# Kernel optimization log

Measured on AMD Instinct MI355X. Metric: run time of the kernel, lower is better.

The kernel has to match this reference:

```python
import jax, jax.numpy as jnp
import numpy as np

silu = jax.nn.silu
B, L, H, IN = 128, 2048, 8, 37
NL = 8  # 4 encoder + 4 decoder SE3 layers, stacked


def _se3_layer(h, pos, eW1, eb1, eW2, eb2, pW1, pb1, pW2, nW1, nb1, nW2, nb2):
    # chain graph: row = 0..N-2, col = 1..N-1 (as in the torch arange edges)
    rel = pos[1:] - pos[:-1]                      # [N-1, 3]
    dist = jnp.linalg.norm(rel, axis=-1, keepdims=True)
    ef = jnp.concatenate([h[:-1], h[1:], dist], axis=-1)   # [N-1, 2H+1]
    ea = silu(ef @ eW1 + eb1) @ eW2 + eb2                   # edge_mlp
    dp = silu(ea @ pW1 + pb1) @ pW2                         # pos_mlp (no bias on last)
    pos_upd = jnp.zeros_like(pos).at[:-1].add(dp).at[1:].add(-dp)
    node_upd = jnp.zeros_like(h).at[:-1].add(ea).at[1:].add(ea)
    h_out = silu(jnp.concatenate([h, node_upd], axis=-1) @ nW1 + nb1) @ nW2 + nb2
    return h_out, pos + 0.1 * pos_upd


def setup_inputs() -> dict:
    key = jax.random.key(0)
    ks = jax.random.split(key, 64)
    i = iter(range(64))
    def p(shape, s=0.1):
        return (jax.random.normal(ks[next(i)], shape, jnp.float32) * s)
    inp = {
        "atom_positions": jax.random.normal(ks[next(i)], (B, L, IN, 3), jnp.float32),
        "atom_mask": (jax.random.uniform(ks[next(i)], (B, L, IN)) < 0.8).astype(jnp.float32),
        "emb_W": p((IN, H)), "emb_b": p((H,)),
        "posemb_W1": p((3, H)), "posemb_b1": p((H,)),
        "posemb_W2": p((H, H)), "posemb_b2": p((H,)),
        # stacked SE3 conv params: layers 0-3 encoder, 4-7 decoder
        "conv_eW1": p((NL, 2 * H + 1, H)), "conv_eb1": p((NL, H)),
        "conv_eW2": p((NL, H, H)), "conv_eb2": p((NL, H)),
        "conv_pW1": p((NL, H, H)), "conv_pb1": p((NL, H)),
        "conv_pW2": p((NL, H, 3)),
        "conv_nW1": p((NL, 2 * H, H)), "conv_nb1": p((NL, H)),
        "conv_nW2": p((NL, H, H)), "conv_nb2": p((NL, H)),
        "tol_W1": p((H, H)), "tol_b1": p((H,)),
        "tol_W2": p((H, H)), "tol_b2": p((H,)),
        "froml_W1": p((H, H)), "froml_b1": p((H,)),
        "froml_W2": p((H, H)), "froml_b2": p((H,)),
        "posdec_W1": p((H, 2 * H)), "posdec_b1": p((2 * H,)),
        "posdec_W2": p((2 * H, IN * 3)), "posdec_b2": p((IN * 3,)),
        "maskdec_W": p((H, IN)), "maskdec_b": p((IN,)),
    }
    return inp


def reference(atom_positions, atom_mask, emb_W, emb_b, posemb_W1, posemb_b1,
              posemb_W2, posemb_b2, conv_eW1, conv_eb1, conv_eW2, conv_eb2,
              conv_pW1, conv_pb1, conv_pW2, conv_nW1, conv_nb1, conv_nW2,
              conv_nb2, tol_W1, tol_b1, tol_W2, tol_b2, froml_W1, froml_b1,
              froml_W2, froml_b2, posdec_W1, posdec_b1, posdec_W2, posdec_b2,
              maskdec_W, maskdec_b):
    # ---- encode ----
    h = atom_mask @ emb_W + emb_b                              # [B,L,H]
    m = atom_mask[..., None]
    mean_pos = (atom_positions * m).sum(axis=2) / (m.sum(axis=2) + 1e-8)  # [B,L,3]
    pos_feat = silu(mean_pos @ posemb_W1 + posemb_b1) @ posemb_W2 + posemb_b2
    h = (h + pos_feat).reshape(B * L, H)
    pos = mean_pos.reshape(B * L, 3)
    for li in range(4):
        h, pos = _se3_layer(h, pos, conv_eW1[li], conv_eb1[li], conv_eW2[li],
                            conv_eb2[li], conv_pW1[li], conv_pb1[li], conv_pW2[li],
                            conv_nW1[li], conv_nb1[li], conv_nW2[li], conv_nb2[li])
    h = h.reshape(B, L, H)
    z = silu(h @ tol_W1 + tol_b1) @ tol_W2 + tol_b2            # [B,L,latent]
    # ---- decode ----
    h = silu(z @ froml_W1 + froml_b1) @ froml_W2 + froml_b2
    h = h.reshape(B * L, H)
    pos = pos  # already flat [B*L, 3]
    for li in range(4, 8):
        h, pos = _se3_layer(h, pos, conv_eW1[li], conv_eb1[li], conv_eW2[li],
                            conv_eb2[li], conv_pW1[li], conv_pb1[li], conv_pW2[li],
                            conv_nW1[li], conv_nb1[li], conv_nW2[li], conv_nb2[li])
    h = h.reshape(B, L, H)
    pos_out = (silu(h @ posdec_W1 + posdec_b1) @ posdec_W2 + posdec_b2)
    pos_out = pos_out.reshape(B, L, IN, 3)
    mask_out = h @ maskdec_W + maskdec_b                       # [B,L,IN]
    return pos_out, mask_out
```

## Files before the change

### kernel.cpp

```cpp
#include <hip/hip_runtime.h>

#define NTOT 262144
#define NLAY 8
#define SEGOUT 48
#define NSEG ((NTOT + SEGOUT - 1) / SEGOUT)

__device__ __forceinline__ float silu_f(float x) {
    return x * __builtin_amdgcn_rcpf(1.0f + __expf(-x));
}

__global__ __launch_bounds__(256) void k_encode(
    const float* __restrict__ ap, const float* __restrict__ amask,
    const float* __restrict__ embW, const float* __restrict__ embB,
    const float* __restrict__ peW1, const float* __restrict__ peB1,
    const float* __restrict__ peW2, const float* __restrict__ peB2,
    float* __restrict__ h0, float* __restrict__ pos0)
{
    __shared__ alignas(16) float sM[64 * 37];
    __shared__ alignas(16) float sA[64 * 111];
    __shared__ alignas(16) float sW[37 * 8];
    const int tid = threadIdx.x;
    const long nb = (long)blockIdx.x * 64;

    if (tid < 74) ((float4*)sW)[tid] = ((const float4*)embW)[tid];
    const float4* gm = (const float4*)(amask + nb * 37);
    float4* sm4 = (float4*)sM;
    #pragma unroll 1
    for (int i = tid; i < 64 * 37 / 4; i += 256) sm4[i] = gm[i];
    const float4* ga = (const float4*)(ap + nb * 111);
    float4* sa4 = (float4*)sA;
    #pragma unroll 1
    for (int i = tid; i < 64 * 111 / 4; i += 256) sa4[i] = ga[i];
    __syncthreads();

    const int n = tid >> 2;
    const int p = tid & 3;
    const int k0 = p * 10;
    const int k1 = (p == 3) ? 37 : k0 + 10;

    const float* mrow = sM + n * 37;
    const float* arow = sA + n * 111;
    float hacc[8] = {0, 0, 0, 0, 0, 0, 0, 0};
    float ps0 = 0.f, ps1 = 0.f, ps2 = 0.f, msum = 0.f;
    #pragma unroll 1
    for (int k = k0; k < k1; ++k) {
        float mv = mrow[k];
        msum += mv;
        const float4* wr = (const float4*)(sW + k * 8);
        float4 w0 = wr[0], w1 = wr[1];
        hacc[0] += mv * w0.x; hacc[1] += mv * w0.y;
        hacc[2] += mv * w0.z; hacc[3] += mv * w0.w;
        hacc[4] += mv * w1.x; hacc[5] += mv * w1.y;
        hacc[6] += mv * w1.z; hacc[7] += mv * w1.w;
        ps0 += mv * arow[k * 3 + 0];
        ps1 += mv * arow[k * 3 + 1];
        ps2 += mv * arow[k * 3 + 2];
    }
    #pragma unroll
    for (int m = 1; m <= 2; m <<= 1) {
        msum += __shfl_xor(msum, m);
        ps0 += __shfl_xor(ps0, m);
        ps1 += __shfl_xor(ps1, m);
        ps2 += __shfl_xor(ps2, m);
        #pragma unroll
        for (int j = 0; j < 8; ++j) hacc[j] += __shfl_xor(hacc[j], m);
    }

    float inv = __builtin_amdgcn_rcpf(msum + 1e-8f);
    float mp0 = ps0 * inv, mp1 = ps1 * inv, mp2 = ps2 * inv;
    float q[8];
    #pragma unroll
    for (int j = 0; j < 8; ++j) {
        float a = peB1[j];
        a += mp0 * peW1[0 * 8 + j];
        a += mp1 * peW1[1 * 8 + j];
        a += mp2 * peW1[2 * 8 + j];
        q[j] = silu_f(a);
    }
    #pragma unroll
    for (int j = 0; j < 8; ++j) {
        float a = peB2[j] + embB[j];
        #pragma unroll
        for (int r = 0; r < 8; ++r) a += q[r] * peW2[r * 8 + j];
        hacc[j] += a;
    }
    const long g = nb + n;
    if (p == 0) ((float4*)(h0 + g * 8))[0] = make_float4(hacc[0], hacc[1], hacc[2], hacc[3]);
    if (p == 1) ((float4*)(h0 + g * 8))[1] = make_float4(hacc[4], hacc[5], hacc[6], hacc[7]);
    if (p == 2) ((float4*)pos0)[g] = make_float4(mp0, mp1, mp2, 0.f);
}


__device__ __forceinline__ void edge_mlp(
    const float* __restrict__ wE1, const float* __restrict__ bE1,
    const float* __restrict__ wE2, const float* __restrict__ bE2,
    const float* __restrict__ wP1, const float* __restrict__ bP1,
    const float* __restrict__ wP2,
    const float* hl, const float* hr, float r0, float r1, float r2,
    float* ea, float& dp0, float& dp1, float& dp2)
{
    float dist = __builtin_amdgcn_sqrtf(r0 * r0 + r1 * r1 + r2 * r2);
    float t1[8];
    #pragma unroll
    for (int j = 0; j < 8; ++j) {
        float a = bE1[j];
        #pragma unroll
        for (int r = 0; r < 8; ++r) a += hl[r] * wE1[r * 8 + j];
        #pragma unroll
        for (int r = 0; r < 8; ++r) a += hr[r] * wE1[64 + r * 8 + j];
        a += dist * wE1[128 + j];
        t1[j] = silu_f(a);
    }
    #pragma unroll
    for (int j = 0; j < 8; ++j) {
        float a = bE2[j];
        #pragma unroll
        for (int r = 0; r < 8; ++r) a += t1[r] * wE2[r * 8 + j];
        ea[j] = a;
    }
    float q[8];
    #pragma unroll
    for (int j = 0; j < 8; ++j) {
        float a = bP1[j];
        #pragma unroll
        for (int r = 0; r < 8; ++r) a += ea[r] * wP1[r * 8 + j];
        q[j] = silu_f(a);
    }
    dp0 = 0.f; dp1 = 0.f; dp2 = 0.f;
    #pragma unroll
    for (int r = 0; r < 8; ++r) {
        dp0 += q[r] * wP2[r * 3 + 0];
        dp1 += q[r] * wP2[r * 3 + 1];
        dp2 += q[r] * wP2[r * 3 + 2];
    }
}

__device__ __forceinline__ void node_mlp(
    const float* __restrict__ wN1, const float* __restrict__ bN1,
    const float* __restrict__ wN2, const float* __restrict__ bN2,
    const float* hl, const float* nu, float* hn)
{
    float u[8];
    #pragma unroll
    for (int j = 0; j < 8; ++j) {
        float a = bN1[j];
        #pragma unroll
        for (int r = 0; r < 8; ++r) a += hl[r] * wN1[r * 8 + j];
        #pragma unroll
        for (int r = 0; r < 8; ++r) a += nu[r] * wN1[64 + r * 8 + j];
        u[j] = silu_f(a);
    }
    #pragma unroll
    for (int j = 0; j < 8; ++j) {
        float a = bN2[j];
        #pragma unroll
        for (int r = 0; r < 8; ++r) a += u[r] * wN2[r * 8 + j];
        hn[j] = a;
    }
}

__device__ __forceinline__ void latent_mlp(
    const float* __restrict__ tW1, const float* __restrict__ tB1,
    const float* __restrict__ tW2, const float* __restrict__ tB2,
    const float* __restrict__ fW1, const float* __restrict__ fB1,
    const float* __restrict__ fW2, const float* __restrict__ fB2,
    float* hn)
{
    float a8[8];
    #pragma unroll
    for (int j = 0; j < 8; ++j) {
        float a = tB1[j];
        #pragma unroll
        for (int r = 0; r < 8; ++r) a += hn[r] * tW1[r * 8 + j];
        a8[j] = silu_f(a);
    }
    float zz[8];
    #pragma unroll
    for (int j = 0; j < 8; ++j) {
        float a = tB2[j];
        #pragma unroll
        for (int r = 0; r < 8; ++r) a += a8[r] * tW2[r * 8 + j];
        zz[j] = a;
    }
    float b8[8];
    #pragma unroll
    for (int j = 0; j < 8; ++j) {
        float a = fB1[j];
        #pragma unroll
        for (int r = 0; r < 8; ++r) a += zz[r] * fW1[r * 8 + j];
        b8[j] = silu_f(a);
    }
    #pragma unroll
    for (int j = 0; j < 8; ++j) {
        float a = fB2[j];
        #pragma unroll
        for (int r = 0; r < 8; ++r) a += b8[r] * fW2[r * 8 + j];
        hn[j] = a;
    }
}

__global__ __launch_bounds__(256) void k_stack(
    const float* __restrict__ h0, const float* __restrict__ pos0,
    float* __restrict__ hfin,
    const float* __restrict__ ceW1, const float* __restrict__ ceB1,
    const float* __restrict__ ceW2, const float* __restrict__ ceB2,
    const float* __restrict__ cpW1, const float* __restrict__ cpB1,
    const float* __restrict__ cpW2,
    const float* __restrict__ cnW1, const float* __restrict__ cnB1,
    const float* __restrict__ cnW2, const float* __restrict__ cnB2,
    const float* __restrict__ tW1, const float* __restrict__ tB1,
    const float* __restrict__ tW2, const float* __restrict__ tB2,
    const float* __restrict__ fW1, const float* __restrict__ fB1,
    const float* __restrict__ fW2, const float* __restrict__ fB2)
{
    const int lane = threadIdx.x & 63;
    const int seg  = blockIdx.x * 4 + (threadIdx.x >> 6);
    const int base = seg * SEGOUT - 8;
    const int n    = base + lane;

    float h[8] = {0, 0, 0, 0, 0, 0, 0, 0};
    float p0 = 0.f, p1 = 0.f, p2 = 0.f;
    if (n >= 0 && n < NTOT) {
        const float4* hp = (const float4*)(h0 + (long)n * 8);
        float4 a = hp[0], b = hp[1];
        h[0] = a.x; h[1] = a.y; h[2] = a.z; h[3] = a.w;
        h[4] = b.x; h[5] = b.y; h[6] = b.z; h[7] = b.w;
        float4 p = ((const float4*)pos0)[n];
        p0 = p.x; p1 = p.y; p2 = p.z;
    }

    const bool eR = (n >= 0) && (n + 1 < NTOT);
    const bool eL = (n >= 1) && (n < NTOT);

    #pragma unroll 1
    for (int li = 0; li < NLAY; ++li) {
        const float* wE1 = ceW1 + li * 136;
        const float* bE1 = ceB1 + li * 8;
        const float* wE2 = ceW2 + li * 64;
        const float* bE2 = ceB2 + li * 8;
        const float* wP1 = cpW1 + li * 64;
        const float* bP1 = cpB1 + li * 8;
        const float* wP2 = cpW2 + li * 24;
        const float* wN1 = cnW1 + li * 128;
        const float* bN1 = cnB1 + li * 8;
        const float* wN2 = cnW2 + li * 64;
        const float* bN2 = cnB2 + li * 8;

        float hr[8], pr0, pr1, pr2;
        #pragma unroll
        for (int j = 0; j < 8; ++j) hr[j] = __shfl_down(h[j], 1);
        pr0 = __shfl_down(p0, 1);
        pr1 = __shfl_down(p1, 1);
        pr2 = __shfl_down(p2, 1);

        float ea[8], dp0, dp1, dp2;
        edge_mlp(wE1, bE1, wE2, bE2, wP1, bP1, wP2,
                 h, hr, pr0 - p0, pr1 - p1, pr2 - p2, ea, dp0, dp1, dp2);

        float eaL[8], dl0, dl1, dl2;
        #pragma unroll
        for (int j = 0; j < 8; ++j) eaL[j] = __shfl_up(ea[j], 1);
        dl0 = __shfl_up(dp0, 1);
        dl1 = __shfl_up(dp1, 1);
        dl2 = __shfl_up(dp2, 1);

        float nu[8];
        #pragma unroll
        for (int j = 0; j < 8; ++j)
            nu[j] = (eR ? ea[j] : 0.f) + (eL ? eaL[j] : 0.f);
        float pu0 = (eR ? dp0 : 0.f) - (eL ? dl0 : 0.f);
        float pu1 = (eR ? dp1 : 0.f) - (eL ? dl1 : 0.f);
        float pu2 = (eR ? dp2 : 0.f) - (eL ? dl2 : 0.f);

        float hn[8];
        node_mlp(wN1, bN1, wN2, bN2, h, nu, hn);

        p0 += 0.1f * pu0; p1 += 0.1f * pu1; p2 += 0.1f * pu2;

        if (li == 3) {
            latent_mlp(tW1, tB1, tW2, tB2, fW1, fB1, fW2, fB2, hn);
        }

        #pragma unroll
        for (int j = 0; j < 8; ++j) h[j] = hn[j];
    }

    if (lane >= 8 && lane < 56 && n < NTOT) {
        float4* hd = (float4*)(hfin + (long)n * 8);
        hd[0] = make_float4(h[0], h[1], h[2], h[3]);
        hd[1] = make_float4(h[4], h[5], h[6], h[7]);
    }
}

__global__ __launch_bounds__(256) void k_decode(
    const float* __restrict__ hfin,
    const float* __restrict__ dW1, const float* __restrict__ dB1,
    const float* __restrict__ dW2, const float* __restrict__ dB2,
    const float* __restrict__ mW, const float* __restrict__ mB,
    float* __restrict__ out)
{
    __shared__ alignas(16) float sh[128 * 8];
    __shared__ alignas(16) float st1[128 * 16];
    const int tid = threadIdx.x;
    const long nb = (long)blockIdx.x * 128;

    ((float4*)sh)[tid] = ((const float4*)(hfin + nb * 8))[tid];
    __syncthreads();

    {
        const int n = tid >> 1;
        const int c0 = (tid & 1) * 8;
        const float4* h4 = (const float4*)(sh + n * 8);
        float4 h0v = h4[0], h1v = h4[1];
        float hr[8] = {h0v.x, h0v.y, h0v.z, h0v.w, h1v.x, h1v.y, h1v.z, h1v.w};
        #pragma unroll
        for (int jj = 0; jj < 8; ++jj) {
            int j = c0 + jj;
            float a = dB1[j];
            #pragma unroll
            for (int r = 0; r < 8; ++r) a += hr[r] * dW1[r * 16 + j];
            st1[n * 16 + j] = silu_f(a);
        }
    }
    __syncthreads();

    if (tid < 222) {
        const int half = (tid >= 111) ? 1 : 0;
        const int j = tid - half * 111;
        float w[16];
        #pragma unroll
        for (int r = 0; r < 16; ++r) w[r] = dW2[r * 111 + j];
        const float bj = dB2[j];
        float* op = out + nb * 111 + j;
        #pragma unroll 2
        for (int n = half; n < 128; n += 2) {
            const float4* t4 = (const float4*)(st1 + n * 16);
            float4 a0 = t4[0], a1 = t4[1], a2 = t4[2], a3 = t4[3];
            float acc = bj;
            acc += a0.x * w[0] + a0.y * w[1] + a0.z * w[2] + a0.w * w[3];
            acc += a1.x * w[4] + a1.y * w[5] + a1.z * w[6] + a1.w * w[7];
            acc += a2.x * w[8] + a2.y * w[9] + a2.z * w[10] + a2.w * w[11];
            acc += a3.x * w[12] + a3.y * w[13] + a3.z * w[14] + a3.w * w[15];
            op[n * 111] = acc;
        }
        const int g6 = tid / 37;
        const int j2 = tid - g6 * 37;
        float wm[8];
        #pragma unroll
        for (int r = 0; r < 8; ++r) wm[r] = mW[r * 37 + j2];
        const float bm = mB[j2];
        float* omp_ = out + (long)NTOT * 111 + nb * 37 + j2;
        #pragma unroll 1
        for (int n = g6; n < 128; n += 6) {
            const float4* h4 = (const float4*)(sh + n * 8);
            float4 h0v = h4[0], h1v = h4[1];
            float acc = bm;
            acc += h0v.x * wm[0] + h0v.y * wm[1] + h0v.z * wm[2] + h0v.w * wm[3];
            acc += h1v.x * wm[4] + h1v.y * wm[5] + h1v.z * wm[6] + h1v.w * wm[7];
            omp_[n * 37] = acc;
        }
    }
}

extern "C" void kernel_launch(void* const* d_in, const int* in_sizes, int n_in,
                              void* d_out, int out_size, void* d_ws, size_t ws_size,
                              hipStream_t stream) {
    const float* ap     = (const float*)d_in[0];
    const float* amask  = (const float*)d_in[1];
    const float* embW   = (const float*)d_in[2];
    const float* embB   = (const float*)d_in[3];
    const float* peW1   = (const float*)d_in[4];
    const float* peB1   = (const float*)d_in[5];
    const float* peW2   = (const float*)d_in[6];
    const float* peB2   = (const float*)d_in[7];
    const float* ceW1   = (const float*)d_in[8];
    const float* ceB1   = (const float*)d_in[9];
    const float* ceW2   = (const float*)d_in[10];
    const float* ceB2   = (const float*)d_in[11];
    const float* cpW1   = (const float*)d_in[12];
    const float* cpB1   = (const float*)d_in[13];
    const float* cpW2   = (const float*)d_in[14];
    const float* cnW1   = (const float*)d_in[15];
    const float* cnB1   = (const float*)d_in[16];
    const float* cnW2   = (const float*)d_in[17];
    const float* cnB2   = (const float*)d_in[18];
    const float* tW1    = (const float*)d_in[19];
    const float* tB1    = (const float*)d_in[20];
    const float* tW2    = (const float*)d_in[21];
    const float* tB2    = (const float*)d_in[22];
    const float* fW1    = (const float*)d_in[23];
    const float* fB1    = (const float*)d_in[24];
    const float* fW2    = (const float*)d_in[25];
    const float* fB2    = (const float*)d_in[26];
    const float* dW1    = (const float*)d_in[27];
    const float* dB1    = (const float*)d_in[28];
    const float* dW2    = (const float*)d_in[29];
    const float* dB2    = (const float*)d_in[30];
    const float* mW     = (const float*)d_in[31];
    const float* mB     = (const float*)d_in[32];

    float* h0   = (float*)d_ws;
    float* pos0 = h0 + (size_t)NTOT * 8;
    float* hfin = pos0 + (size_t)NTOT * 4;
    float* out  = (float*)d_out;

    k_encode<<<NTOT / 64, 256, 0, stream>>>(ap, amask, embW, embB,
                                            peW1, peB1, peW2, peB2, h0, pos0);
    const int nblk = (NSEG + 3) / 4;
    k_stack<<<nblk, 256, 0, stream>>>(
        h0, pos0, hfin,
        ceW1, ceB1, ceW2, ceB2, cpW1, cpB1, cpW2,
        cnW1, cnB1, cnW2, cnB2,
        tW1, tB1, tW2, tB2, fW1, fB1, fW2, fB2);
    k_decode<<<NTOT / 128, 256, 0, stream>>>(hfin, dW1, dB1, dW2, dB2, mW, mB, out);
}
```

Measured before the change: 432.4 us.

## Fuse encode, SE3 layer stack and decode into a single kernel

Merges the three kernels into one. Each wave now computes the atom-mask embedding and mean position for its 64-node window, including halo nodes, by staging mask and position chunks through per-wave shared memory. After the layer stack it runs the position and mask decoders on its 48 owned nodes from shared memory. This drops the global round trips for h0, pos0 and hfin and two kernel launches. In exchange the halo nodes' input rows are read and encoded redundantly, the encode runs in eight serialized chunks with block barriers, and global loads become scalar instead of float4.

Measured after the change: 598.7 us. 1.38x slower.

```diff
diff --git a/kernel.cpp b/kernel.cpp
--- a/kernel.cpp
+++ b/kernel.cpp
@@ -4,92 +4,11 @@
 #define NLAY 8
 #define SEGOUT 48
 #define NSEG ((NTOT + SEGOUT - 1) / SEGOUT)
+#define NBLK ((NSEG + 3) / 4)
 
 __device__ __forceinline__ float silu_f(float x) {
     return x * __builtin_amdgcn_rcpf(1.0f + __expf(-x));
 }
-
-__global__ __launch_bounds__(256) void k_encode(
-    const float* __restrict__ ap, const float* __restrict__ amask,
-    const float* __restrict__ embW, const float* __restrict__ embB,
-    const float* __restrict__ peW1, const float* __restrict__ peB1,
-    const float* __restrict__ peW2, const float* __restrict__ peB2,
-    float* __restrict__ h0, float* __restrict__ pos0)
-{
-    __shared__ alignas(16) float sM[64 * 37];
-    __shared__ alignas(16) float sA[64 * 111];
-    __shared__ alignas(16) float sW[37 * 8];
-    const int tid = threadIdx.x;
-    const long nb = (long)blockIdx.x * 64;
-
-    if (tid < 74) ((float4*)sW)[tid] = ((const float4*)embW)[tid];
-    const float4* gm = (const float4*)(amask + nb * 37);
-    float4* sm4 = (float4*)sM;
-    #pragma unroll 1
-    for (int i = tid; i < 64 * 37 / 4; i += 256) sm4[i] = gm[i];
-    const float4* ga = (const float4*)(ap + nb * 111);
-    float4* sa4 = (float4*)sA;
-    #pragma unroll 1
-    for (int i = tid; i < 64 * 111 / 4; i += 256) sa4[i] = ga[i];
-    __syncthreads();
-
-    const int n = tid >> 2;
-    const int p = tid & 3;
-    const int k0 = p * 10;
-    const int k1 = (p == 3) ? 37 : k0 + 10;
-
-    const float* mrow = sM + n * 37;
-    const float* arow = sA + n * 111;
-    float hacc[8] = {0, 0, 0, 0, 0, 0, 0, 0};
-    float ps0 = 0.f, ps1 = 0.f, ps2 = 0.f, msum = 0.f;
-    #pragma unroll 1
-    for (int k = k0; k < k1; ++k) {
-        float mv = mrow[k];
-        msum += mv;
-        const float4* wr = (const float4*)(sW + k * 8);
-        float4 w0 = wr[0], w1 = wr[1];
-        hacc[0] += mv * w0.x; hacc[1] += mv * w0.y;
-        hacc[2] += mv * w0.z; hacc[3] += mv * w0.w;
-        hacc[4] += mv * w1.x; hacc[5] += mv * w1.y;
-        hacc[6] += mv * w1.z; hacc[7] += mv * w1.w;
-        ps0 += mv * arow[k * 3 + 0];
-        ps1 += mv * arow[k * 3 + 1];
-        ps2 += mv * arow[k * 3 + 2];
-    }
-    #pragma unroll
-    for (int m = 1; m <= 2; m <<= 1) {
-        msum += __shfl_xor(msum, m);
-        ps0 += __shfl_xor(ps0, m);
-        ps1 += __shfl_xor(ps1, m);
-        ps2 += __shfl_xor(ps2, m);
-        #pragma unroll
-        for (int j = 0; j < 8; ++j) hacc[j] += __shfl_xor(hacc[j], m);
-    }
-
-    float inv = __builtin_amdgcn_rcpf(msum + 1e-8f);
-    float mp0 = ps0 * inv, mp1 = ps1 * inv, mp2 = ps2 * inv;
-    float q[8];
-    #pragma unroll
-    for (int j = 0; j < 8; ++j) {
-        float a = peB1[j];
-        a += mp0 * peW1[0 * 8 + j];
-        a += mp1 * peW1[1 * 8 + j];
-        a += mp2 * peW1[2 * 8 + j];
-        q[j] = silu_f(a);
-    }
-    #pragma unroll
-    for (int j = 0; j < 8; ++j) {
-        float a = peB2[j] + embB[j];
-        #pragma unroll
-        for (int r = 0; r < 8; ++r) a += q[r] * peW2[r * 8 + j];
-        hacc[j] += a;
-    }
-    const long g = nb + n;
-    if (p == 0) ((float4*)(h0 + g * 8))[0] = make_float4(hacc[0], hacc[1], hacc[2], hacc[3]);
-    if (p == 1) ((float4*)(h0 + g * 8))[1] = make_float4(hacc[4], hacc[5], hacc[6], hacc[7]);
-    if (p == 2) ((float4*)pos0)[g] = make_float4(mp0, mp1, mp2, 0.f);
-}
-
 
 __device__ __forceinline__ void edge_mlp(
     const float* __restrict__ wE1, const float* __restrict__ bE1,
@@ -199,9 +118,11 @@
     }
 }
 
-__global__ __launch_bounds__(256) void k_stack(
-    const float* __restrict__ h0, const float* __restrict__ pos0,
-    float* __restrict__ hfin,
+__global__ __launch_bounds__(256) void k_fused(
+    const float* __restrict__ ap, const float* __restrict__ amask,
+    const float* __restrict__ embW, const float* __restrict__ embB,
+    const float* __restrict__ peW1, const float* __restrict__ peB1,
+    const float* __restrict__ peW2, const float* __restrict__ peB2,
     const float* __restrict__ ceW1, const float* __restrict__ ceB1,
     const float* __restrict__ ceW2, const float* __restrict__ ceB2,
     const float* __restrict__ cpW1, const float* __restrict__ cpB1,
@@ -211,22 +132,104 @@
     const float* __restrict__ tW1, const float* __restrict__ tB1,
     const float* __restrict__ tW2, const float* __restrict__ tB2,
     const float* __restrict__ fW1, const float* __restrict__ fB1,
-    const float* __restrict__ fW2, const float* __restrict__ fB2)
+    const float* __restrict__ fW2, const float* __restrict__ fB2,
+    const float* __restrict__ dW1, const float* __restrict__ dB1,
+    const float* __restrict__ dW2, const float* __restrict__ dB2,
+    const float* __restrict__ mW, const float* __restrict__ mB,
+    float* __restrict__ out)
 {
-    const int lane = threadIdx.x & 63;
-    const int seg  = blockIdx.x * 4 + (threadIdx.x >> 6);
+    __shared__ alignas(16) float smem[4736];
+    const int tid  = threadIdx.x;
+    const int w    = tid >> 6;
+    const int lane = tid & 63;
+    const int seg  = blockIdx.x * 4 + w;
     const int base = seg * SEGOUT - 8;
     const int n    = base + lane;
 
-    float h[8] = {0, 0, 0, 0, 0, 0, 0, 0};
+    float* stg = smem + w * 1184;
+    float h[8];
     float p0 = 0.f, p1 = 0.f, p2 = 0.f;
-    if (n >= 0 && n < NTOT) {
-        const float4* hp = (const float4*)(h0 + (long)n * 8);
-        float4 a = hp[0], b = hp[1];
-        h[0] = a.x; h[1] = a.y; h[2] = a.z; h[3] = a.w;
-        h[4] = b.x; h[5] = b.y; h[6] = b.z; h[7] = b.w;
-        float4 p = ((const float4*)pos0)[n];
-        p0 = p.x; p1 = p.y; p2 = p.z;
+    const int nic  = lane >> 3;
+    const int part = lane & 7;
+    const int k0   = (part < 5) ? part * 5 : 25 + (part - 5) * 4;
+    const int kc   = (part < 5) ? 5 : 4;
+
+    #pragma unroll 1
+    for (int c = 0; c < 8; ++c) {
+        const int n0 = base + c * 8;
+        const long gm0 = (long)n0 * 37;
+        #pragma unroll 1
+        for (int i = lane; i < 296; i += 64) {
+            long gi = gm0 + i;
+            stg[i] = (gi >= 0 && gi < (long)NTOT * 37) ? amask[gi] : 0.f;
+        }
+        const long gp0 = (long)n0 * 111;
+        #pragma unroll 1
+        for (int i = lane; i < 888; i += 64) {
+            long gi = gp0 + i;
+            stg[296 + i] = (gi >= 0 && gi < (long)NTOT * 111) ? ap[gi] : 0.f;
+        }
+        __syncthreads();
+
+        const float* mrow = stg + nic * 37;
+        const float* arow = stg + 296 + nic * 111;
+        float hacc[8] = {0, 0, 0, 0, 0, 0, 0, 0};
+        float ps0 = 0.f, ps1 = 0.f, ps2 = 0.f, msum = 0.f;
+        #pragma unroll 1
+        for (int kk = 0; kk < kc; ++kk) {
+            const int k = k0 + kk;
+            float mv = mrow[k];
+            msum += mv;
+            const float4* wr = (const float4*)(embW + k * 8);
+            float4 w0 = wr[0], w1 = wr[1];
+            hacc[0] += mv * w0.x; hacc[1] += mv * w0.y;
+            hacc[2] += mv * w0.z; hacc[3] += mv * w0.w;
+            hacc[4] += mv * w1.x; hacc[5] += mv * w1.y;
+            hacc[6] += mv * w1.z; hacc[7] += mv * w1.w;
+            ps0 += mv * arow[k * 3 + 0];
+            ps1 += mv * arow[k * 3 + 1];
+            ps2 += mv * arow[k * 3 + 2];
+        }
+        #pragma unroll
+        for (int m = 1; m <= 4; m <<= 1) {
+            msum += __shfl_xor(msum, m);
+            ps0 += __shfl_xor(ps0, m);
+            ps1 += __shfl_xor(ps1, m);
+            ps2 += __shfl_xor(ps2, m);
+            #pragma unroll
+            for (int j = 0; j < 8; ++j) hacc[j] += __shfl_xor(hacc[j], m);
+        }
+        float inv = __builtin_amdgcn_rcpf(msum + 1e-8f);
+        float mp0 = ps0 * inv, mp1 = ps1 * inv, mp2 = ps2 * inv;
+        float q[8];
+        #pragma unroll
+        for (int j = 0; j < 8; ++j) {
+            float a = peB1[j];
+            a += mp0 * peW1[0 * 8 + j];
+            a += mp1 * peW1[1 * 8 + j];
+            a += mp2 * peW1[2 * 8 + j];
+            q[j] = silu_f(a);
+        }
+        float hv[8];
+        #pragma unroll
+        for (int j = 0; j < 8; ++j) {
+            float a = peB2[j] + embB[j];
+            #pragma unroll
+            for (int r = 0; r < 8; ++r) a += q[r] * peW2[r * 8 + j];
+            hv[j] = hacc[j] + a;
+        }
+        #pragma unroll
+        for (int j = 0; j < 8; ++j) {
+            float v = __shfl(hv[j], part * 8);
+            if (nic == c) h[j] = v;
+        }
+        {
+            float v0 = __shfl(mp0, part * 8);
+            float v1 = __shfl(mp1, part * 8);
+            float v2 = __shfl(mp2, part * 8);
+            if (nic == c) { p0 = v0; p1 = v1; p2 = v2; }
+        }
+        __syncthreads();
     }
 
     const bool eR = (n >= 0) && (n + 1 < NTOT);
@@ -285,63 +288,56 @@
         for (int j = 0; j < 8; ++j) h[j] = hn[j];
     }
 
-    if (lane >= 8 && lane < 56 && n < NTOT) {
-        float4* hd = (float4*)(hfin + (long)n * 8);
-        hd[0] = make_float4(h[0], h[1], h[2], h[3]);
-        hd[1] = make_float4(h[4], h[5], h[6], h[7]);
-    }
-}
-
-__global__ __launch_bounds__(256) void k_decode(
-    const float* __restrict__ hfin,
-    const float* __restrict__ dW1, const float* __restrict__ dB1,
-    const float* __restrict__ dW2, const float* __restrict__ dB2,
-    const float* __restrict__ mW, const float* __restrict__ mB,
-    float* __restrict__ out)
-{
-    __shared__ alignas(16) float sh[128 * 8];
-    __shared__ alignas(16) float st1[128 * 16];
-    const int tid = threadIdx.x;
-    const long nb = (long)blockIdx.x * 128;
-
-    ((float4*)sh)[tid] = ((const float4*)(hfin + nb * 8))[tid];
+    float* sh  = smem;
+    float* st1 = smem + 192 * 8;
+    if (lane >= 8 && lane < 56) {
+        const int row = w * 48 + (lane - 8);
+        float4* d = (float4*)(sh + row * 8);
+        d[0] = make_float4(h[0], h[1], h[2], h[3]);
+        d[1] = make_float4(h[4], h[5], h[6], h[7]);
+    }
     __syncthreads();
 
     {
-        const int n = tid >> 1;
         const int c0 = (tid & 1) * 8;
-        const float4* h4 = (const float4*)(sh + n * 8);
-        float4 h0v = h4[0], h1v = h4[1];
-        float hr[8] = {h0v.x, h0v.y, h0v.z, h0v.w, h1v.x, h1v.y, h1v.z, h1v.w};
-        #pragma unroll
-        for (int jj = 0; jj < 8; ++jj) {
-            int j = c0 + jj;
-            float a = dB1[j];
+        #pragma unroll 1
+        for (int nn = tid >> 1; nn < 192; nn += 128) {
+            const float4* h4 = (const float4*)(sh + nn * 8);
+            float4 h0v = h4[0], h1v = h4[1];
+            float hr8[8] = {h0v.x, h0v.y, h0v.z, h0v.w, h1v.x, h1v.y, h1v.z, h1v.w};
             #pragma unroll
-            for (int r = 0; r < 8; ++r) a += hr[r] * dW1[r * 16 + j];
-            st1[n * 16 + j] = silu_f(a);
+            for (int jj = 0; jj < 8; ++jj) {
+                int j = c0 + jj;
+                float a = dB1[j];
+                #pragma unroll
+                for (int r = 0; r < 8; ++r) a += hr8[r] * dW1[r * 16 + j];
+                st1[nn * 16 + j] = silu_f(a);
+            }
         }
     }
     __syncthreads();
 
+    const long nb = (long)blockIdx.x * 192;
     if (tid < 222) {
         const int half = (tid >= 111) ? 1 : 0;
         const int j = tid - half * 111;
-        float w[16];
-        #pragma unroll
-        for (int r = 0; r < 16; ++r) w[r] = dW2[r * 111 + j];
+        float wv[16];
+        #pragma unroll
+        for (int r = 0; r < 16; ++r) wv[r] = dW2[r * 111 + j];
         const float bj = dB2[j];
         float* op = out + nb * 111 + j;
         #pragma unroll 2
-        for (int n = half; n < 128; n += 2) {
-            const float4* t4 = (const float4*)(st1 + n * 16);
-            float4 a0 = t4[0], a1 = t4[1], a2 = t4[2], a3 = t4[3];
-            float acc = bj;
-            acc += a0.x * w[0] + a0.y * w[1] + a0.z * w[2] + a0.w * w[3];
-            acc += a1.x * w[4] + a1.y * w[5] + a1.z * w[6] + a1.w * w[7];
-            acc += a2.x * w[8] + a2.y * w[9] + a2.z * w[10] + a2.w * w[11];
-            acc += a3.x * w[12] + a3.y * w[13] + a3.z * w[14] + a3.w * w[15];
-            op[n * 111] = acc;
+        for (int nn = half; nn < 192; nn += 2) {
+            if (nb + nn < NTOT) {
+                const float4* t4 = (const float4*)(st1 + nn * 16);
+                float4 a0 = t4[0], a1 = t4[1], a2 = t4[2], a3 = t4[3];
+                float acc = bj;
+                acc += a0.x * wv[0]  + a0.y * wv[1]  + a0.z * wv[2]  + a0.w * wv[3];
+                acc += a1.x * wv[4]  + a1.y * wv[5]  + a1.z * wv[6]  + a1.w * wv[7];
+                acc += a2.x * wv[8]  + a2.y * wv[9]  + a2.z * wv[10] + a2.w * wv[11];
+                acc += a3.x * wv[12] + a3.y * wv[13] + a3.z * wv[14] + a3.w * wv[15];
+                op[(long)nn * 111] = acc;
+            }
         }
         const int g6 = tid / 37;
         const int j2 = tid - g6 * 37;
@@ -351,13 +347,15 @@
         const float bm = mB[j2];
         float* omp_ = out + (long)NTOT * 111 + nb * 37 + j2;
         #pragma unroll 1
-        for (int n = g6; n < 128; n += 6) {
-            const float4* h4 = (const float4*)(sh + n * 8);
-            float4 h0v = h4[0], h1v = h4[1];
-            float acc = bm;
-            acc += h0v.x * wm[0] + h0v.y * wm[1] + h0v.z * wm[2] + h0v.w * wm[3];
-            acc += h1v.x * wm[4] + h1v.y * wm[5] + h1v.z * wm[6] + h1v.w * wm[7];
-            omp_[n * 37] = acc;
+        for (int nn = g6; nn < 192; nn += 6) {
+            if (nb + nn < NTOT) {
+                const float4* h4 = (const float4*)(sh + nn * 8);
+                float4 h0v = h4[0], h1v = h4[1];
+                float acc = bm;
+                acc += h0v.x * wm[0] + h0v.y * wm[1] + h0v.z * wm[2] + h0v.w * wm[3];
+                acc += h1v.x * wm[4] + h1v.y * wm[5] + h1v.z * wm[6] + h1v.w * wm[7];
+                omp_[(long)nn * 37] = acc;
+            }
         }
     }
 }
@@ -399,18 +397,13 @@
     const float* mW     = (const float*)d_in[31];
     const float* mB     = (const float*)d_in[32];
 
-    float* h0   = (float*)d_ws;
-    float* pos0 = h0 + (size_t)NTOT * 8;
-    float* hfin = pos0 + (size_t)NTOT * 4;
-    float* out  = (float*)d_out;
-
-    k_encode<<<NTOT / 64, 256, 0, stream>>>(ap, amask, embW, embB,
-                                            peW1, peB1, peW2, peB2, h0, pos0);
-    const int nblk = (NSEG + 3) / 4;
-    k_stack<<<nblk, 256, 0, stream>>>(
-        h0, pos0, hfin,
+    float* out = (float*)d_out;
+    (void)d_ws; (void)ws_size;
+
+    k_fused<<<NBLK, 256, 0, stream>>>(
+        ap, amask, embW, embB, peW1, peB1, peW2, peB2,
         ceW1, ceB1, ceW2, ceB2, cpW1, cpB1, cpW2,
         cnW1, cnB1, cnW2, cnB2,
-        tW1, tB1, tW2, tB2, fW1, fB1, fW2, fB2);
-    k_decode<<<NTOT / 128, 256, 0, stream>>>(hfin, dW1, dB1, dW2, dB2, mW, mB, out);
-}
+        tW1, tB1, tW2, tB2, fW1, fB1, fW2, fB2,
+        dW1, dB1, dW2, dB2, mW, mB, out);
+}
```

## Fuse decoder output heads into SE3 stack kernel via shared memory

Applied to the files above, without the earlier changes.

Merges the separate decode kernel into the layer-stack kernel. Each block stages its 192 final node features in shared memory, then computes the position and mask output heads directly, so the hfin round trip through global memory and one kernel launch go away. It also replaces the boundary select logic with float mask multiplies. The cost is extra shared memory per stack block, which may lower occupancy, and the output writes now use the stack's segment-based tiling with bounds checks.

Measured after the change: 471.9 us. 1.09x slower.

```diff
diff --git a/kernel.cpp b/kernel.cpp
--- a/kernel.cpp
+++ b/kernel.cpp
@@ -4,6 +4,7 @@
 #define NLAY 8
 #define SEGOUT 48
 #define NSEG ((NTOT + SEGOUT - 1) / SEGOUT)
+#define NBLK ((NSEG + 3) / 4)
 
 __device__ __forceinline__ float silu_f(float x) {
     return x * __builtin_amdgcn_rcpf(1.0f + __expf(-x));
@@ -90,7 +91,6 @@
     if (p == 2) ((float4*)pos0)[g] = make_float4(mp0, mp1, mp2, 0.f);
 }
 
-
 __device__ __forceinline__ void edge_mlp(
     const float* __restrict__ wE1, const float* __restrict__ bE1,
     const float* __restrict__ wE2, const float* __restrict__ bE2,
@@ -199,9 +199,8 @@
     }
 }
 
-__global__ __launch_bounds__(256) void k_stack(
+__global__ __launch_bounds__(256) void k_stackdec(
     const float* __restrict__ h0, const float* __restrict__ pos0,
-    float* __restrict__ hfin,
     const float* __restrict__ ceW1, const float* __restrict__ ceB1,
     const float* __restrict__ ceW2, const float* __restrict__ ceB2,
     const float* __restrict__ cpW1, const float* __restrict__ cpB1,
@@ -211,10 +210,17 @@
     const float* __restrict__ tW1, const float* __restrict__ tB1,
     const float* __restrict__ tW2, const float* __restrict__ tB2,
     const float* __restrict__ fW1, const float* __restrict__ fB1,
-    const float* __restrict__ fW2, const float* __restrict__ fB2)
+    const float* __restrict__ fW2, const float* __restrict__ fB2,
+    const float* __restrict__ dW1, const float* __restrict__ dB1,
+    const float* __restrict__ dW2, const float* __restrict__ dB2,
+    const float* __restrict__ mW, const float* __restrict__ mB,
+    float* __restrict__ out)
 {
-    const int lane = threadIdx.x & 63;
-    const int seg  = blockIdx.x * 4 + (threadIdx.x >> 6);
+    __shared__ alignas(16) float smem[192 * 24];
+    const int tid  = threadIdx.x;
+    const int w    = tid >> 6;
+    const int lane = tid & 63;
+    const int seg  = blockIdx.x * 4 + w;
     const int base = seg * SEGOUT - 8;
     const int n    = base + lane;
 
@@ -229,8 +235,8 @@
         p0 = p.x; p1 = p.y; p2 = p.z;
     }
 
-    const bool eR = (n >= 0) && (n + 1 < NTOT);
-    const bool eL = (n >= 1) && (n < NTOT);
+    const float mR = ((n >= 0) && (n + 1 < NTOT)) ? 1.f : 0.f;
+    const float mL = ((n >= 1) && (n < NTOT)) ? 1.f : 0.f;
 
     #pragma unroll 1
     for (int li = 0; li < NLAY; ++li) {
@@ -267,10 +273,10 @@
         float nu[8];
         #pragma unroll
         for (int j = 0; j < 8; ++j)
-            nu[j] = (eR ? ea[j] : 0.f) + (eL ? eaL[j] : 0.f);
-        float pu0 = (eR ? dp0 : 0.f) - (eL ? dl0 : 0.f);
-        float pu1 = (eR ? dp1 : 0.f) - (eL ? dl1 : 0.f);
-        float pu2 = (eR ? dp2 : 0.f) - (eL ? dl2 : 0.f);
+            nu[j] = mR * ea[j] + mL * eaL[j];
+        float pu0 = mR * dp0 - mL * dl0;
+        float pu1 = mR * dp1 - mL * dl1;
+        float pu2 = mR * dp2 - mL * dl2;
 
         float hn[8];
         node_mlp(wN1, bN1, wN2, bN2, h, nu, hn);
@@ -285,63 +291,56 @@
         for (int j = 0; j < 8; ++j) h[j] = hn[j];
     }
 
-    if (lane >= 8 && lane < 56 && n < NTOT) {
-        float4* hd = (float4*)(hfin + (long)n * 8);
-        hd[0] = make_float4(h[0], h[1], h[2], h[3]);
-        hd[1] = make_float4(h[4], h[5], h[6], h[7]);
-    }
-}
-
-__global__ __launch_bounds__(256) void k_decode(
-    const float* __restrict__ hfin,
-    const float* __restrict__ dW1, const float* __restrict__ dB1,
-    const float* __restrict__ dW2, const float* __restrict__ dB2,
-    const float* __restrict__ mW, const float* __restrict__ mB,
-    float* __restrict__ out)
-{
-    __shared__ alignas(16) float sh[128 * 8];
-    __shared__ alignas(16) float st1[128 * 16];
-    const int tid = threadIdx.x;
-    const long nb = (long)blockIdx.x * 128;
-
-    ((float4*)sh)[tid] = ((const float4*)(hfin + nb * 8))[tid];
+    float* sh  = smem;
+    float* st1 = smem + 192 * 8;
+    if (lane >= 8 && lane < 56) {
+        const int row = w * 48 + (lane - 8);
+        float4* d = (float4*)(sh + row * 8);
+        d[0] = make_float4(h[0], h[1], h[2], h[3]);
+        d[1] = make_float4(h[4], h[5], h[6], h[7]);
+    }
     __syncthreads();
 
     {
-        const int n = tid >> 1;
         const int c0 = (tid & 1) * 8;
-        const float4* h4 = (const float4*)(sh + n * 8);
-        float4 h0v = h4[0], h1v = h4[1];
-        float hr[8] = {h0v.x, h0v.y, h0v.z, h0v.w, h1v.x, h1v.y, h1v.z, h1v.w};
-        #pragma unroll
-        for (int jj = 0; jj < 8; ++jj) {
-            int j = c0 + jj;
-            float a = dB1[j];
+        #pragma unroll 1
+        for (int nn = tid >> 1; nn < 192; nn += 128) {
+            const float4* h4 = (const float4*)(sh + nn * 8);
+            float4 h0v = h4[0], h1v = h4[1];
+            float hr8[8] = {h0v.x, h0v.y, h0v.z, h0v.w, h1v.x, h1v.y, h1v.z, h1v.w};
             #pragma unroll
-            for (int r = 0; r < 8; ++r) a += hr[r] * dW1[r * 16 + j];
-            st1[n * 16 + j] = silu_f(a);
+            for (int jj = 0; jj < 8; ++jj) {
+                int j = c0 + jj;
+                float a = dB1[j];
+                #pragma unroll
+                for (int r = 0; r < 8; ++r) a += hr8[r] * dW1[r * 16 + j];
+                st1[nn * 16 + j] = silu_f(a);
+            }
         }
     }
     __syncthreads();
 
+    const long nb = (long)blockIdx.x * 192;
     if (tid < 222) {
         const int half = (tid >= 111) ? 1 : 0;
         const int j = tid - half * 111;
-        float w[16];
-        #pragma unroll
-        for (int r = 0; r < 16; ++r) w[r] = dW2[r * 111 + j];
+        float wv[16];
+        #pragma unroll
+        for (int r = 0; r < 16; ++r) wv[r] = dW2[r * 111 + j];
         const float bj = dB2[j];
         float* op = out + nb * 111 + j;
         #pragma unroll 2
-        for (int n = half; n < 128; n += 2) {
-            const float4* t4 = (const float4*)(st1 + n * 16);
-            float4 a0 = t4[0], a1 = t4[1], a2 = t4[2], a3 = t4[3];
-            float acc = bj;
-            acc += a0.x * w[0] + a0.y * w[1] + a0.z * w[2] + a0.w * w[3];
-            acc += a1.x * w[4] + a1.y * w[5] + a1.z * w[6] + a1.w * w[7];
-            acc += a2.x * w[8] + a2.y * w[9] + a2.z * w[10] + a2.w * w[11];
-            acc += a3.x * w[12] + a3.y * w[13] + a3.z * w[14] + a3.w * w[15];
-            op[n * 111] = acc;
+        for (int nn = half; nn < 192; nn += 2) {
+            if (nb + nn < NTOT) {
+                const float4* t4 = (const float4*)(st1 + nn * 16);
+                float4 a0 = t4[0], a1 = t4[1], a2 = t4[2], a3 = t4[3];
+                float acc = bj;
+                acc += a0.x * wv[0]  + a0.y * wv[1]  + a0.z * wv[2]  + a0.w * wv[3];
+                acc += a1.x * wv[4]  + a1.y * wv[5]  + a1.z * wv[6]  + a1.w * wv[7];
+                acc += a2.x * wv[8]  + a2.y * wv[9]  + a2.z * wv[10] + a2.w * wv[11];
+                acc += a3.x * wv[12] + a3.y * wv[13] + a3.z * wv[14] + a3.w * wv[15];
+                op[(long)nn * 111] = acc;
+            }
         }
         const int g6 = tid / 37;
         const int j2 = tid - g6 * 37;
@@ -351,13 +350,15 @@
         const float bm = mB[j2];
         float* omp_ = out + (long)NTOT * 111 + nb * 37 + j2;
         #pragma unroll 1
-        for (int n = g6; n < 128; n += 6) {
-            const float4* h4 = (const float4*)(sh + n * 8);
-            float4 h0v = h4[0], h1v = h4[1];
-            float acc = bm;
-            acc += h0v.x * wm[0] + h0v.y * wm[1] + h0v.z * wm[2] + h0v.w * wm[3];
-            acc += h1v.x * wm[4] + h1v.y * wm[5] + h1v.z * wm[6] + h1v.w * wm[7];
-            omp_[n * 37] = acc;
+        for (int nn = g6; nn < 192; nn += 6) {
+            if (nb + nn < NTOT) {
+                const float4* h4 = (const float4*)(sh + nn * 8);
+                float4 h0v = h4[0], h1v = h4[1];
+                float acc = bm;
+                acc += h0v.x * wm[0] + h0v.y * wm[1] + h0v.z * wm[2] + h0v.w * wm[3];
+                acc += h1v.x * wm[4] + h1v.y * wm[5] + h1v.z * wm[6] + h1v.w * wm[7];
+                omp_[(long)nn * 37] = acc;
+            }
         }
     }
 }
@@ -388,10 +389,10 @@
     const float* tB1    = (const float*)d_in[20];
     const float* tW2    = (const float*)d_in[21];
     const float* tB2    = (const float*)d_in[22];
-    const float* fW1    = (const float*)d_in[23];
-    const float* fB1    = (const float*)d_in[24];
-    const float* fW2    = (const float*)d_in[25];
-    const float* fB2    = (const float*)d_in[26];
+    const float* froW1  = (const float*)d_in[23];
+    const float* froB1  = (const float*)d_in[24];
+    const float* froW2  = (const float*)d_in[25];
+    const float* froB2  = (const float*)d_in[26];
     const float* dW1    = (const float*)d_in[27];
     const float* dB1    = (const float*)d_in[28];
     const float* dW2    = (const float*)d_in[29];
@@ -401,16 +402,14 @@
 
     float* h0   = (float*)d_ws;
     float* pos0 = h0 + (size_t)NTOT * 8;
-    float* hfin = pos0 + (size_t)NTOT * 4;
     float* out  = (float*)d_out;
 
     k_encode<<<NTOT / 64, 256, 0, stream>>>(ap, amask, embW, embB,
                                             peW1, peB1, peW2, peB2, h0, pos0);
-    const int nblk = (NSEG + 3) / 4;
-    k_stack<<<nblk, 256, 0, stream>>>(
-        h0, pos0, hfin,
+    k_stackdec<<<NBLK, 256, 0, stream>>>(
+        h0, pos0,
         ceW1, ceB1, ceW2, ceB2, cpW1, cpB1, cpW2,
         cnW1, cnB1, cnW2, cnB2,
-        tW1, tB1, tW2, tB2, fW1, fB1, fW2, fB2);
-    k_decode<<<NTOT / 128, 256, 0, stream>>>(hfin, dW1, dB1, dW2, dB2, mW, mB, out);
-}
+        tW1, tB1, tW2, tB2, froW1, froB1, froW2, froB2,
+        dW1, dB1, dW2, dB2, mW, mB, out);
+}
```

## Split 8-layer stack into two 4-layer kernels with smaller halos

Applied to the files above, without the earlier changes.

The fused 8-layer chain kernel used an 8-node halo per side, so each 64-lane wave produced only 48 outputs. The stack is now split into two launches of 4 layers each, with a 4-node halo and 56 outputs per wave. This cuts redundant halo computation. In exchange it adds an extra launch and a global round trip of h and pos between the encoder and decoder halves.

Measured after the change: 449.6 us. 4.0% more time.

```diff
diff --git a/kernel.cpp b/kernel.cpp
--- a/kernel.cpp
+++ b/kernel.cpp
@@ -2,8 +2,9 @@
 
 #define NTOT 262144
 #define NLAY 8
-#define SEGOUT 48
-#define NSEG ((NTOT + SEGOUT - 1) / SEGOUT)
+#define SEG4 56
+#define NSEG4 ((NTOT + SEG4 - 1) / SEG4)
+#define NBLK4 ((NSEG4 + 3) / 4)
 
 __device__ __forceinline__ float silu_f(float x) {
     return x * __builtin_amdgcn_rcpf(1.0f + __expf(-x));
@@ -90,7 +91,6 @@
     if (p == 2) ((float4*)pos0)[g] = make_float4(mp0, mp1, mp2, 0.f);
 }
 
-
 __device__ __forceinline__ void edge_mlp(
     const float* __restrict__ wE1, const float* __restrict__ bE1,
     const float* __restrict__ wE2, const float* __restrict__ bE2,
@@ -199,9 +199,10 @@
     }
 }
 
-__global__ __launch_bounds__(256) void k_stack(
-    const float* __restrict__ h0, const float* __restrict__ pos0,
-    float* __restrict__ hfin,
+__global__ __launch_bounds__(256) void k_stack4(
+    const float* __restrict__ hin, const float* __restrict__ pin,
+    float* __restrict__ hout, float* __restrict__ pout,
+    const int l0, const int do_latent, const int do_pos,
     const float* __restrict__ ceW1, const float* __restrict__ ceB1,
     const float* __restrict__ ceW2, const float* __restrict__ ceB2,
     const float* __restrict__ cpW1, const float* __restrict__ cpB1,
@@ -215,17 +216,17 @@
 {
     const int lane = threadIdx.x & 63;
     const int seg  = blockIdx.x * 4 + (threadIdx.x >> 6);
-    const int base = seg * SEGOUT - 8;
+    const int base = seg * SEG4 - 4;
     const int n    = base + lane;
 
     float h[8] = {0, 0, 0, 0, 0, 0, 0, 0};
     float p0 = 0.f, p1 = 0.f, p2 = 0.f;
     if (n >= 0 && n < NTOT) {
-        const float4* hp = (const float4*)(h0 + (long)n * 8);
+        const float4* hp = (const float4*)(hin + (long)n * 8);
         float4 a = hp[0], b = hp[1];
         h[0] = a.x; h[1] = a.y; h[2] = a.z; h[3] = a.w;
         h[4] = b.x; h[5] = b.y; h[6] = b.z; h[7] = b.w;
-        float4 p = ((const float4*)pos0)[n];
+        float4 p = ((const float4*)pin)[n];
         p0 = p.x; p1 = p.y; p2 = p.z;
     }
 
@@ -233,7 +234,8 @@
     const bool eL = (n >= 1) && (n < NTOT);
 
     #pragma unroll 1
-    for (int li = 0; li < NLAY; ++li) {
+    for (int ii = 0; ii < 4; ++ii) {
+        const int li = l0 + ii;
         const float* wE1 = ceW1 + li * 136;
         const float* bE1 = ceB1 + li * 8;
         const float* wE2 = ceW2 + li * 64;
@@ -277,7 +279,7 @@
 
         p0 += 0.1f * pu0; p1 += 0.1f * pu1; p2 += 0.1f * pu2;
 
-        if (li == 3) {
+        if (do_latent && li == 3) {
             latent_mlp(tW1, tB1, tW2, tB2, fW1, fB1, fW2, fB2, hn);
         }
 
@@ -285,10 +287,11 @@
         for (int j = 0; j < 8; ++j) h[j] = hn[j];
     }
 
-    if (lane >= 8 && lane < 56 && n < NTOT) {
-        float4* hd = (float4*)(hfin + (long)n * 8);
+    if (lane >= 4 && lane < 60 && n < NTOT) {
+        float4* hd = (float4*)(hout + (long)n * 8);
         hd[0] = make_float4(h[0], h[1], h[2], h[3]);
         hd[1] = make_float4(h[4], h[5], h[6], h[7]);
+        if (do_pos) ((float4*)pout)[n] = make_float4(p0, p1, p2, 0.f);
     }
 }
 
@@ -399,16 +402,22 @@
     const float* mW     = (const float*)d_in[31];
     const float* mB     = (const float*)d_in[32];
 
-    float* h0   = (float*)d_ws;
-    float* pos0 = h0 + (size_t)NTOT * 8;
-    float* hfin = pos0 + (size_t)NTOT * 4;
-    float* out  = (float*)d_out;
+    float* h0     = (float*)d_ws;
+    float* pos0   = h0 + (size_t)NTOT * 8;
+    float* hmid   = pos0 + (size_t)NTOT * 4;
+    float* posmid = hmid + (size_t)NTOT * 8;
+    float* hfin   = h0;
+    float* out    = (float*)d_out;
 
     k_encode<<<NTOT / 64, 256, 0, stream>>>(ap, amask, embW, embB,
                                             peW1, peB1, peW2, peB2, h0, pos0);
-    const int nblk = (NSEG + 3) / 4;
-    k_stack<<<nblk, 256, 0, stream>>>(
-        h0, pos0, hfin,
+    k_stack4<<<NBLK4, 256, 0, stream>>>(
+        h0, pos0, hmid, posmid, 0, 1, 1,
+        ceW1, ceB1, ceW2, ceB2, cpW1, cpB1, cpW2,
+        cnW1, cnB1, cnW2, cnB2,
+        tW1, tB1, tW2, tB2, fW1, fB1, fW2, fB2);
+    k_stack4<<<NBLK4, 256, 0, stream>>>(
+        hmid, posmid, hfin, posmid, 4, 0, 0,
         ceW1, ceB1, ceW2, ceB2, cpW1, cpB1, cpW2,
         cnW1, cnB1, cnW2, cnB2,
         tW1, tB1, tW2, tB2, fW1, fB1, fW2, fB2);
```
